# Performance work log

Hardware: AMD Instinct MI355X
Metric: run time of the kernel (lower is better)

## Reference

```python
import jax, jax.numpy as jnp
import numpy as np

B, L, D, H, S = 4, 4096, 1024, 16, 4
DH = D // H


def setup_inputs() -> dict:
    key = jax.random.key(0)
    ks = jax.random.split(key, 12)
    std = 0.02
    inp = {
        "x": jax.random.normal(ks[0], (B, L, D), jnp.float32),
        "scale_logits": jax.random.normal(ks[1], (S,), jnp.float32),
        "wq": jax.random.normal(ks[2], (D, D), jnp.float32) * std,
        "bq": jnp.zeros((D,), jnp.float32),
        "wk": jax.random.normal(ks[3], (D, D), jnp.float32) * std,
        "bk": jnp.zeros((D,), jnp.float32),
        "wv": jax.random.normal(ks[4], (D, D), jnp.float32) * std,
        "bv": jnp.zeros((D,), jnp.float32),
        "wo": jax.random.normal(ks[5], (D, D), jnp.float32) * std,
        "bo": jnp.zeros((D,), jnp.float32),
        "ws": jax.random.normal(ks[6], (S, D, D), jnp.float32) * std,  # per-scale Linear weights (out,in)
        "bs": jax.random.normal(ks[7], (S, D), jnp.float32) * std,
    }
    return inp


def reference(x, scale_logits, wq, bq, wk, bk, wv, bv, wo, bo, ws, bs):
    # q/k/v projections; kept flat (B,L,D) since the torch code re-flattens before scale proj
    qf = x @ wq.T + bq
    kf = x @ wk.T + bk
    vf = x @ wv.T + bv
    # per-scale linear projection, vectorized over scales: (B,S,L,D)
    sq = jnp.einsum('bld,sed->bsle', qf, ws) + bs[None, :, None, :]
    sk = jnp.einsum('bld,sed->bsle', kf, ws) + bs[None, :, None, :]
    sv = jnp.einsum('bld,sed->bsle', vf, ws) + bs[None, :, None, :]
    sq = sq.reshape(B, S, L, H, DH)
    sk = sk.reshape(B, S, L, H, DH)
    sv = sv.reshape(B, S, L, H, DH)
    # faithful to torch: matmul over last two dims of (B,L,H,dh) -> per-position
    # head-mixing scores of shape (B,S,L,H,H)
    scale = 1.0 / np.sqrt(DH).astype(np.float32)
    scores = jnp.einsum('bslhd,bslgd->bslhg', sq, sk) * scale
    attn = jax.nn.softmax(scores, axis=-1)
    out = jnp.einsum('bslhg,bslgd->bslhd', attn, sv)  # (B,S,L,H,DH)
    w = jax.nn.softmax(scale_logits, axis=0)  # (S,)
    combined = jnp.einsum('s,bslhd->blhd', w, out).reshape(B, L, D)
    return combined @ wo.T + bo
```

## Files before the change

### kernel.cpp

```cpp
#include <hip/hip_runtime.h>


typedef unsigned short u16;
typedef __attribute__((ext_vector_type(8))) short s16x8;
typedef __attribute__((ext_vector_type(8))) unsigned short u16x8;
typedef __attribute__((ext_vector_type(4))) float f32x4;

#define MM 16384
#define DDIM 1024
#define DDSQ 1048576ull

__device__ __forceinline__ u16 f2bf(float f) {
  unsigned u = __float_as_uint(f);
  u = (u + 0x7FFFu + ((u >> 16) & 1u)) >> 16;
  return (u16)u;
}
__device__ __forceinline__ float b2f(u16 b) {
  return __uint_as_float(((unsigned)b) << 16);
}
__device__ __forceinline__ void gload_lds16(const void* g, void* l) {
  __builtin_amdgcn_global_load_lds(
      (const __attribute__((address_space(1))) void*)g,
      (__attribute__((address_space(3))) void*)l, 16, 0, 0);
}

__global__ __launch_bounds__(256) void k_f32_to_bf16(
    const float* __restrict__ in, u16* __restrict__ out, int n4) {
  int i = blockIdx.x * 256 + threadIdx.x;
  if (i >= n4) return;
  float4 v = reinterpret_cast<const float4*>(in)[i];
  ushort4 o;
  o.x = f2bf(v.x); o.y = f2bf(v.y); o.z = f2bf(v.z); o.w = f2bf(v.w);
  reinterpret_cast<ushort4*>(out)[i] = o;
}

__global__ __launch_bounds__(256) void k_transpose_bf16(
    const float* __restrict__ wq, const float* __restrict__ wk,
    const float* __restrict__ wv, u16* __restrict__ out) {
  __shared__ float tile[32][33];
  const float* src = (blockIdx.z == 0) ? wq : (blockIdx.z == 1) ? wk : wv;
  u16* dst = out + (size_t)blockIdx.z * DDSQ;
  int tx = threadIdx.x, ty = threadIdx.y;
  int bx = blockIdx.x * 32, by = blockIdx.y * 32;
#pragma unroll
  for (int i = 0; i < 4; ++i)
    tile[ty + 8 * i][tx] = src[(size_t)(by + ty + 8 * i) * DDIM + bx + tx];
  __syncthreads();
#pragma unroll
  for (int i = 0; i < 4; ++i)
    dst[(size_t)(bx + ty + 8 * i) * DDIM + by + tx] = f2bf(tile[tx][ty + 8 * i]);
}

__global__ __launch_bounds__(256) void k_bias_fuse(
    const float* __restrict__ ws, const float* __restrict__ bq,
    const float* __restrict__ bk, const float* __restrict__ bv,
    const float* __restrict__ bs, float* __restrict__ bf) {
  int idx = blockIdx.y;
  int s = idx / 3, t = idx - s * 3;
  const float* bt = (t == 0) ? bq : (t == 1) ? bk : bv;
  int lane = threadIdx.x & 63, wid = threadIdx.x >> 6;
  int e = blockIdx.x * 4 + wid;
  const float* wr = ws + (size_t)s * DDSQ + (size_t)e * DDIM;
  float p = 0.f;
  for (int j = lane; j < DDIM; j += 64) p += wr[j] * bt[j];
#pragma unroll
  for (int off = 32; off > 0; off >>= 1) p += __shfl_xor(p, off);
  if (lane == 0) bf[idx * DDIM + e] = p + bs[s * DDIM + e];
}

template <typename OutT>
__global__ __launch_bounds__(256) void k_gemm_bt(
    const u16* __restrict__ A, const u16* __restrict__ B, OutT* __restrict__ C,
    const float* __restrict__ bias, int M, int N, int K,
    size_t za, size_t zb, size_t zc, size_t zbias, int zmode) {
  __shared__ u16 lds_a[128 * 32];
  __shared__ u16 lds_b[128 * 32];

  int z = blockIdx.x >> 3;
  int n_blk = blockIdx.x & 7;
  int m_blk = blockIdx.y;
  if (zmode == 1) { A += (size_t)(z / 3) * za; B += (size_t)(z % 3) * zb; }
  else            { A += (size_t)z * za;       B += (size_t)z * zb; }
  C += (size_t)z * zc;
  const float* biasz = bias ? (bias + (size_t)z * zbias) : nullptr;

  int m0 = m_blk * 128, n0 = n_blk * 128;
  int tid = threadIdx.x;
  int lane = tid & 63, wid = tid >> 6;
  int wm = wid >> 1, wn = wid & 1;

  f32x4 acc[4][4] = {};

  auto stage = [&](int k0) {
#pragma unroll
    for (int i = 0; i < 2; ++i) {
      int c = wid * 2 + i;
      int row = c * 16 + (lane >> 2);
      int col = (lane & 3) * 8;
      gload_lds16(A + (size_t)(m0 + row) * K + k0 + col, &lds_a[c * 512]);
      gload_lds16(B + (size_t)(n0 + row) * K + k0 + col, &lds_b[c * 512]);
    }
  };

  stage(0);
  int ar = (wm * 64 + (lane & 15)) * 32 + (lane >> 4) * 8;
  int br = (wn * 64 + (lane & 15)) * 32 + (lane >> 4) * 8;
  for (int k0 = 0;;) {
    __syncthreads();
    s16x8 af[4], bfr[4];
#pragma unroll
    for (int mi = 0; mi < 4; ++mi)
      af[mi] = *reinterpret_cast<const s16x8*>(&lds_a[ar + mi * 16 * 32]);
#pragma unroll
    for (int ni = 0; ni < 4; ++ni)
      bfr[ni] = *reinterpret_cast<const s16x8*>(&lds_b[br + ni * 16 * 32]);
#pragma unroll
    for (int mi = 0; mi < 4; ++mi)
#pragma unroll
      for (int ni = 0; ni < 4; ++ni)
        acc[mi][ni] = __builtin_amdgcn_mfma_f32_16x16x32_bf16(
            af[mi], bfr[ni], acc[mi][ni], 0, 0, 0);
    k0 += 32;
    if (k0 >= K) break;
    __syncthreads();
    stage(k0);
  }

#pragma unroll
  for (int mi = 0; mi < 4; ++mi) {
#pragma unroll
    for (int ni = 0; ni < 4; ++ni) {
      int colg = n0 + wn * 64 + ni * 16 + (lane & 15);
      float badd = biasz ? biasz[colg] : 0.f;
#pragma unroll
      for (int r = 0; r < 4; ++r) {
        int rowg = m0 + wm * 64 + mi * 16 + ((lane >> 4) << 2) + r;
        float v = acc[mi][ni][r] + badd;
        if constexpr (sizeof(OutT) == 2) C[(size_t)rowg * N + colg] = f2bf(v);
        else                             C[(size_t)rowg * N + colg] = v;
      }
    }
  }
}

template <typename OutT>
__global__ __launch_bounds__(512, 1) void k_gemm256(
    const u16* __restrict__ A, const u16* __restrict__ B, OutT* __restrict__ C,
    const float* __restrict__ bias, int M, int N, int K,
    size_t za, size_t zb, size_t zc, size_t zbias, int nbx) {
  __shared__ u16 lds[4][2][8192];

  int z = blockIdx.x / nbx;
  int nb = blockIdx.x - z * nbx;
  const u16* Ag = A + (size_t)z * za;
  const u16* Bg = B + (size_t)z * zb;
  OutT* Cg = C + (size_t)z * zc;
  const float* biasz = bias + (size_t)z * zbias;

  int m0 = blockIdx.y * 256, n0 = nb * 256;
  int tid = threadIdx.x;
  int lane = tid & 63, wid = tid >> 6;
  int wm = wid >> 2, wn = wid & 3;
  int NT = K >> 5;

  int scb = ((lane & 3) * 16) ^ (((lane >> 3) & 3) << 4);
  const char* srcA[2]; const char* srcB[2]; int ldsc[2];
#pragma unroll
  for (int r = 0; r < 2; ++r) {
    int c = r * 8 + wid;
    int row = c * 16 + (lane >> 2);
    srcA[r] = (const char*)Ag + ((size_t)(m0 + row) * K) * 2 + scb;
    srcB[r] = (const char*)Bg + ((size_t)(n0 + row) * K) * 2 + scb;
    ldsc[r] = c * 1024;
  }
  char* lbase = (char*)&lds[0][0][0];

  int fxor = ((lane >> 4) * 16) ^ (((lane >> 1) & 3) << 4);
  int aoff = (wm * 128 + (lane & 15)) * 64 + fxor;
  int boff = (wn * 64 + (lane & 15)) * 64 + fxor;

  f32x4 acc[8][4] = {};
  s16x8 cA0[4], cA1[4], cB[4];
  s16x8 nA0[4], nA1[4], nB[4];

#define STAGE_A(kt, rg)                                                   \
  {                                                                       \
    _Pragma("unroll") for (int r = 0; r < 2; ++r)                         \
        gload_lds16(srcA[r] + (size_t)(kt) * 64,                          \
                    lbase + (rg) * 32768 + ldsc[r]);                      \
  }
#define STAGE_B(kt, rg)                                                   \
  {                                                                       \
    _Pragma("unroll") for (int r = 0; r < 2; ++r)                         \
        gload_lds16(srcB[r] + (size_t)(kt) * 64,                          \
                    lbase + (rg) * 32768 + 16384 + ldsc[r]);              \
  }
#define SUBITER(C0, C1, CBv, N0, N1, NBv, tcur)                           \
  {                                                                       \
    asm volatile("s_waitcnt vmcnt(4)" ::: "memory");                      \
    asm volatile("s_barrier" ::: "memory");                               \
    int tn = (tcur) + 1 < NT ? (tcur) + 1 : NT - 1;                       \
    const char* bA = lbase + (tn & 3) * 32768;                            \
    const char* bB = bA + 16384;                                          \
    _Pragma("unroll") for (int i = 0; i < 4; ++i)                         \
        NBv[i] = *(const s16x8*)(bB + boff + i * 1024);                   \
    _Pragma("unroll") for (int i = 0; i < 4; ++i)                         \
        N0[i] = *(const s16x8*)(bA + aoff + i * 1024);                    \
    _Pragma("unroll") for (int i = 0; i < 4; ++i)                         \
        N1[i] = *(const s16x8*)(bA + aoff + 4096 + i * 1024);             \
    int ts = (tcur) + 3 < NT ? (tcur) + 3 : NT - 1;                       \
    int rgs = ((tcur) + 3) & 3;                                           \
    STAGE_A(ts, rgs); STAGE_B(ts, rgs);                                   \
    __builtin_amdgcn_s_setprio(1);                                        \
    _Pragma("unroll") for (int mi = 0; mi < 4; ++mi)                      \
      _Pragma("unroll") for (int ni = 0; ni < 4; ++ni)                    \
          acc[mi][ni] = __builtin_amdgcn_mfma_f32_16x16x32_bf16(          \
              C0[mi], CBv[ni], acc[mi][ni], 0, 0, 0);                     \
    _Pragma("unroll") for (int mi = 0; mi < 4; ++mi)                      \
      _Pragma("unroll") for (int ni = 0; ni < 4; ++ni)                    \
          acc[mi + 4][ni] = __builtin_amdgcn_mfma_f32_16x16x32_bf16(      \
              C1[mi], CBv[ni], acc[mi + 4][ni], 0, 0, 0);                 \
    __builtin_amdgcn_s_setprio(0);                                        \
  }

  STAGE_A(0, 0); STAGE_B(0, 0);
  STAGE_A(1, 1); STAGE_B(1, 1);
  STAGE_A(2, 2); STAGE_B(2, 2);
  asm volatile("s_waitcnt vmcnt(8)" ::: "memory");
  asm volatile("s_barrier" ::: "memory");
  {
    const char* bA = lbase;
    const char* bB = bA + 16384;
#pragma unroll
    for (int i = 0; i < 4; ++i) cB[i]  = *(const s16x8*)(bB + boff + i * 1024);
#pragma unroll
    for (int i = 0; i < 4; ++i) cA0[i] = *(const s16x8*)(bA + aoff + i * 1024);
#pragma unroll
    for (int i = 0; i < 4; ++i)
      cA1[i] = *(const s16x8*)(bA + aoff + 4096 + i * 1024);
  }

  for (int t = 0; t < NT; t += 2) {
    SUBITER(cA0, cA1, cB, nA0, nA1, nB, t);
    SUBITER(nA0, nA1, nB, cA0, cA1, cB, t + 1);
  }
#undef SUBITER
#undef STAGE_A
#undef STAGE_B

  asm volatile("s_waitcnt vmcnt(0)" ::: "memory");

#pragma unroll
  for (int mi = 0; mi < 8; ++mi) {
#pragma unroll
    for (int ni = 0; ni < 4; ++ni) {
      int colg = n0 + wn * 64 + ni * 16 + (lane & 15);
      float badd = biasz[colg];
#pragma unroll
      for (int r = 0; r < 4; ++r) {
        int rowg = m0 + wm * 128 + mi * 16 + ((lane >> 4) << 2) + r;
        float v = acc[mi][ni][r] + badd;
        if constexpr (sizeof(OutT) == 2) Cg[(size_t)rowg * N + colg] = f2bf(v);
        else                             Cg[(size_t)rowg * N + colg] = v;
      }
    }
  }
}

__global__ __launch_bounds__(256) void k_attn_all(
    const u16* __restrict__ proj, u16* __restrict__ outbf,
    const float* __restrict__ sl, int rows) {
  __shared__ u16 kv[4][2][2][1024];
  int lane = threadIdx.x & 63, wid = threadIdx.x >> 6;
  int row = blockIdx.x * 4 + wid;
  int h = lane >> 2, dq = lane & 3;
  int doff = h * 64 + dq * 16;

  float l0 = sl[0], l1 = sl[1], l2 = sl[2], l3 = sl[3];
  float lm = fmaxf(fmaxf(l0, l1), fmaxf(l2, l3));
  float e0 = __expf(l0 - lm), e1 = __expf(l1 - lm), e2 = __expf(l2 - lm),
        e3 = __expf(l3 - lm);
  float esum = e0 + e1 + e2 + e3;
  float wsc4[4] = {e0 / esum, e1 / esum, e2 / esum, e3 / esum};

#define KV_ISSUE(s, buf)                                                   \
  {                                                                        \
    const u16* kr = proj + ((size_t)(3 * (s) + 1) * rows + row) * DDIM;    \
    const u16* vr = proj + ((size_t)(3 * (s) + 2) * rows + row) * DDIM;    \
    gload_lds16(kr + lane * 8,       &kv[wid][buf][0][0]);                 \
    gload_lds16(kr + 512 + lane * 8, &kv[wid][buf][0][512]);               \
    gload_lds16(vr + lane * 8,       &kv[wid][buf][1][0]);                 \
    gload_lds16(vr + 512 + lane * 8, &kv[wid][buf][1][512]);               \
  }

  KV_ISSUE(0, 0);

  float acc[16];
#pragma unroll
  for (int i = 0; i < 16; ++i) acc[i] = 0.f;

  for (int s = 0; s < 4; ++s) {
    int buf = s & 1;

    const u16* qr = proj + ((size_t)(3 * s) * rows + row) * DDIM + doff;
    u16x8 q0 = *reinterpret_cast<const u16x8*>(qr);
    u16x8 q1 = *reinterpret_cast<const u16x8*>(qr + 8);

    if (s < 3) KV_ISSUE(s + 1, buf ^ 1);

    if (s < 3) asm volatile("s_waitcnt vmcnt(6)" ::: "memory");
    else       asm volatile("s_waitcnt vmcnt(0)" ::: "memory");

    float qf[16];
#pragma unroll
    for (int i = 0; i < 8; ++i) {
      qf[i]     = b2f(q0[i]) * 0.125f;
      qf[8 + i] = b2f(q1[i]) * 0.125f;
    }

    float sc[16];
#pragma unroll
    for (int g = 0; g < 16; ++g) {
      const u16* kp = &kv[wid][buf][0][g * 64 + dq * 16];
      u16x8 k0 = *reinterpret_cast<const u16x8*>(kp);
      u16x8 k1 = *reinterpret_cast<const u16x8*>(kp + 8);
      float d = 0.f;
#pragma unroll
      for (int i = 0; i < 8; ++i) d = fmaf(qf[i], b2f(k0[i]), d);
#pragma unroll
      for (int i = 0; i < 8; ++i) d = fmaf(qf[8 + i], b2f(k1[i]), d);
      d += __shfl_xor(d, 1);
      d += __shfl_xor(d, 2);
      sc[g] = d;
    }

    float mx = sc[0];
#pragma unroll
    for (int g = 1; g < 16; ++g) mx = fmaxf(mx, sc[g]);
    float sum = 0.f;
#pragma unroll
    for (int g = 0; g < 16; ++g) { sc[g] = __expf(sc[g] - mx); sum += sc[g]; }
    float inv = wsc4[s] / sum;
#pragma unroll
    for (int g = 0; g < 16; ++g) sc[g] *= inv;

#pragma unroll
    for (int g = 0; g < 16; ++g) {
      float a = sc[g];
      const u16* vp = &kv[wid][buf][1][g * 64 + dq * 16];
      u16x8 v0 = *reinterpret_cast<const u16x8*>(vp);
      u16x8 v1 = *reinterpret_cast<const u16x8*>(vp + 8);
#pragma unroll
      for (int i = 0; i < 8; ++i) {
        acc[i]     = fmaf(a, b2f(v0[i]), acc[i]);
        acc[8 + i] = fmaf(a, b2f(v1[i]), acc[8 + i]);
      }
    }
  }
#undef KV_ISSUE

  u16* op = outbf + (size_t)row * DDIM + doff;
  u16x8 o0, o1;
#pragma unroll
  for (int i = 0; i < 8; ++i) {
    o0[i] = f2bf(acc[i]);
    o1[i] = f2bf(acc[8 + i]);
  }
  *reinterpret_cast<u16x8*>(op) = o0;
  *reinterpret_cast<u16x8*>(op + 8) = o1;
}

extern "C" void kernel_launch(void* const* d_in, const int* in_sizes, int n_in,
                              void* d_out, int out_size, void* d_ws,
                              size_t ws_size, hipStream_t stream) {
  const float* x  = (const float*)d_in[0];
  const float* sl = (const float*)d_in[1];
  const float* wq = (const float*)d_in[2];
  const float* bq = (const float*)d_in[3];
  const float* wk = (const float*)d_in[4];
  const float* bk = (const float*)d_in[5];
  const float* wv = (const float*)d_in[6];
  const float* bv = (const float*)d_in[7];
  const float* wo = (const float*)d_in[8];
  const float* bo = (const float*)d_in[9];
  const float* ws = (const float*)d_in[10];
  const float* bs = (const float*)d_in[11];
  float* out = (float*)d_out;

  char* wsb = (char*)d_ws;
  size_t off = 0;
  u16* xbf    = (u16*)(wsb + off); off += (size_t)MM * DDIM * 2;
  u16* wfus   = (u16*)(wsb + off); off += 12ull * DDSQ * 2;
  u16* wobf   = (u16*)(wsb + off); off += DDSQ * 2;
  float* bfus = (float*)(wsb + off); off += 65536;
  u16* combc  = (u16*)(wsb + off); off += (size_t)MM * DDIM * 2;
  char* dynr  = wsb + off;
  size_t fixed = off;

  int chunk = 4096;
  while (chunk > 1024 && fixed + (size_t)12 * chunk * DDIM * 2 > ws_size)
    chunk >>= 1;
  u16* projc = (u16*)dynr;
  u16* wtT  = (u16*)dynr;
  u16* wsbf = (u16*)(dynr + 3ull * DDSQ * 2);

  int n4;
  n4 = MM * DDIM / 4;
  k_f32_to_bf16<<<(n4 + 255) / 256, 256, 0, stream>>>(x, xbf, n4);
  n4 = (int)(4 * DDSQ / 4);
  k_f32_to_bf16<<<(n4 + 255) / 256, 256, 0, stream>>>(ws, wsbf, n4);
  n4 = (int)(DDSQ / 4);
  k_f32_to_bf16<<<(n4 + 255) / 256, 256, 0, stream>>>(wo, wobf, n4);

  k_transpose_bf16<<<dim3(32, 32, 3), dim3(32, 8), 0, stream>>>(wq, wk, wv, wtT);
  k_bias_fuse<<<dim3(256, 12), 256, 0, stream>>>(ws, bq, bk, bv, bs, bfus);

  k_gemm_bt<u16><<<dim3(96, 8), 256, 0, stream>>>(
      wsbf, wtT, wfus, nullptr, 1024, 1024, 1024, DDSQ, DDSQ, DDSQ, 0, 1);

  int nchunks = MM / chunk;
  for (int c = 0; c < nchunks; ++c) {
    const u16* xa = xbf + (size_t)c * chunk * DDIM;
    k_gemm256<u16><<<dim3(48, chunk / 256), 512, 0, stream>>>(
        xa, wfus, projc, bfus, chunk, 1024, 1024,
        0, DDSQ, (size_t)chunk * DDIM, DDIM, 4);
    k_attn_all<<<dim3(chunk / 4), 256, 0, stream>>>(
        projc, combc + (size_t)c * chunk * DDIM, sl, chunk);
  }

  k_gemm256<float><<<dim3(4, 64), 512, 0, stream>>>(
      combc, wobf, out, bo, MM, 1024, 1024, 0, 0, 0, 0, 4);
}
```

Baseline: 690.0 us.

## Add eight-phase pipelined bf16 GEMM kernel for fused scale projections

Adds a new 256x256-tile bf16 GEMM kernel and uses it for the large fused Q/K/V scale projection GEMM. K is split into half-tiles across double-buffered LDS, with direct global-to-LDS loads for the next tiles issued between the MFMA phases. It also adds explicit barriers, waitcnt, priority bumps around MFMA and XOR-swizzled LDS addressing. The intent is to hide global memory latency behind tensor-core work. The cost is 128KB of LDS per block (one block per CU) and more barriers per K step.

```diff
diff --git a/kernel.cpp b/kernel.cpp
--- a/kernel.cpp
+++ b/kernel.cpp
@@ -267,6 +267,158 @@
   }
 }
 
+__global__ __launch_bounds__(512, 1) void k_gemm8p(
+    const u16* __restrict__ A, const u16* __restrict__ B, u16* __restrict__ C,
+    const float* __restrict__ bias, int M, int N, int K,
+    size_t za, size_t zb, size_t zc, size_t zbias, int nbx) {
+  __shared__ char lds[131072];
+
+  int z = blockIdx.x / nbx;
+  int nb = blockIdx.x - z * nbx;
+  const u16* Ag = A + (size_t)z * za;
+  const u16* Bg = B + (size_t)z * zb;
+  u16* Cg = C + (size_t)z * zc;
+  const float* biasz = bias + (size_t)z * zbias;
+
+  int m0 = blockIdx.y * 256, n0 = nb * 256;
+  int tid = threadIdx.x;
+  int lane = tid & 63, wid = tid >> 6;
+  int wm = wid >> 2, wn = wid & 3;
+  int NT = K >> 6;
+
+  int scb = ((lane & 3) * 16) ^ (((lane >> 3) & 3) << 4);
+  const char* srcA[2]; const char* srcB[2]; int ldsc[2];
+#pragma unroll
+  for (int r = 0; r < 2; ++r) {
+    int c = r * 8 + wid;
+    int row = c * 16 + (lane >> 2);
+    srcA[r] = (const char*)Ag + ((size_t)(m0 + row) * K) * 2 + scb;
+    srcB[r] = (const char*)Bg + ((size_t)(n0 + row) * K) * 2 + scb;
+    ldsc[r] = c * 1024;
+  }
+
+  int fxor = ((lane >> 4) * 16) ^ (((lane >> 1) & 3) << 4);
+  int aoffb = (wm * 128 + (lane & 15)) * 64 + fxor;
+  int boffb = (wn * 64 + (lane & 15)) * 64 + fxor;
+
+  f32x4 acc[2][4][4] = {};
+  s16x8 fb0[4], fb1[4];
+
+#define ST8(srcX, kt, kh, dst)                                            \
+  {                                                                       \
+    _Pragma("unroll") for (int r = 0; r < 2; ++r)                         \
+        gload_lds16(srcX[r] + (size_t)(kt) * 128 + (kh) * 64,             \
+                    lds + (dst) + ldsc[r]);                               \
+  }
+#define BAR8 asm volatile("s_barrier" ::: "memory")
+#define LGKM0                                                             \
+  {                                                                       \
+    asm volatile("s_waitcnt lgkmcnt(0)" ::: "memory");                    \
+    __builtin_amdgcn_sched_barrier(0);                                    \
+  }
+#define RDA8(fa, bo, kh, ch)                                              \
+  {                                                                       \
+    const char* ra_ = lds + (bo) + (kh) * 16384;                          \
+    _Pragma("unroll") for (int mf = 0; mf < 4; ++mf)                      \
+        fa[mf] = *(const s16x8*)(ra_ + aoffb + (ch) * 4096 + mf * 1024);  \
+  }
+#define RDB8(fb, bo, kh)                                                  \
+  {                                                                       \
+    const char* rb_ = lds + (bo) + 32768 + (kh) * 16384;                  \
+    _Pragma("unroll") for (int nf = 0; nf < 4; ++nf)                      \
+        fb[nf] = *(const s16x8*)(rb_ + boffb + nf * 1024);                \
+  }
+#define MFMA16(ch, fa, fb)                                                \
+  {                                                                       \
+    __builtin_amdgcn_s_setprio(1);                                        \
+    _Pragma("unroll") for (int mf = 0; mf < 4; ++mf)                      \
+      _Pragma("unroll") for (int nf = 0; nf < 4; ++nf)                    \
+          acc[ch][mf][nf] = __builtin_amdgcn_mfma_f32_16x16x32_bf16(      \
+              fa[mf], fb[nf], acc[ch][mf][nf], 0, 0, 0);                  \
+    __builtin_amdgcn_s_setprio(0);                                        \
+  }
+
+  ST8(srcA, 0, 0, 0);
+  ST8(srcB, 0, 0, 32768);
+  ST8(srcA, 0, 1, 16384);
+  ST8(srcB, 0, 1, 49152);
+  {
+    int t1 = (NT > 1) ? 1 : 0;
+    ST8(srcA, t1, 0, 65536 + 0);
+    ST8(srcB, t1, 0, 65536 + 32768);
+  }
+  asm volatile("s_waitcnt vmcnt(4)" ::: "memory");
+  BAR8;
+
+  for (int t = 0; t < NT; ++t) {
+    int bo  = (t & 1) << 16;
+    int bo1 = ((t & 1) ^ 1) << 16;
+    int tn1 = (t + 1 < NT) ? t + 1 : NT - 1;
+    int tn2 = (t + 2 < NT) ? t + 2 : NT - 1;
+
+    {
+      s16x8 fa[4];
+      RDB8(fb0, bo, 0);
+      RDA8(fa, bo, 0, 0);
+      ST8(srcA, tn1, 1, bo1 + 16384);
+      BAR8; LGKM0;
+      MFMA16(0, fa, fb0);
+      BAR8;
+    }
+    {
+      s16x8 fa[4];
+      RDA8(fa, bo, 0, 1);
+      ST8(srcB, tn1, 1, bo1 + 49152);
+      BAR8; LGKM0;
+      MFMA16(1, fa, fb0);
+      BAR8;
+    }
+    {
+      s16x8 fa[4];
+      RDB8(fb1, bo, 1);
+      RDA8(fa, bo, 1, 0);
+      ST8(srcA, tn2, 0, bo + 0);
+      BAR8; LGKM0;
+      MFMA16(0, fa, fb1);
+      BAR8;
+    }
+    {
+      s16x8 fa[4];
+      RDA8(fa, bo, 1, 1);
+      ST8(srcB, tn2, 0, bo + 32768);
+      BAR8; LGKM0;
+      MFMA16(1, fa, fb1);
+      asm volatile("s_waitcnt vmcnt(4)" ::: "memory");
+      BAR8;
+    }
+  }
+#undef ST8
+#undef BAR8
+#undef LGKM0
+#undef RDA8
+#undef RDB8
+#undef MFMA16
+
+  asm volatile("s_waitcnt vmcnt(0)" ::: "memory");
+
+#pragma unroll
+  for (int ch = 0; ch < 2; ++ch) {
+#pragma unroll
+    for (int mf = 0; mf < 4; ++mf) {
+#pragma unroll
+      for (int nf = 0; nf < 4; ++nf) {
+        int colg = n0 + wn * 64 + nf * 16 + (lane & 15);
+        float badd = biasz[colg];
+#pragma unroll
+        for (int r = 0; r < 4; ++r) {
+          int rowg = m0 + wm * 128 + ch * 64 + mf * 16 + ((lane >> 4) << 2) + r;
+          Cg[(size_t)rowg * N + colg] = f2bf(acc[ch][mf][nf][r] + badd);
+        }
+      }
+    }
+  }
+}
+
 __global__ __launch_bounds__(256) void k_attn_all(
     const u16* __restrict__ proj, u16* __restrict__ outbf,
     const float* __restrict__ sl, int rows) {
@@ -421,7 +573,7 @@
   int nchunks = MM / chunk;
   for (int c = 0; c < nchunks; ++c) {
     const u16* xa = xbf + (size_t)c * chunk * DDIM;
-    k_gemm256<u16><<<dim3(48, chunk / 256), 512, 0, stream>>>(
+    k_gemm8p<<<dim3(48, chunk / 256), 512, 0, stream>>>(
         xa, wfus, projc, bfus, chunk, 1024, 1024,
         0, DDSQ, (size_t)chunk * DDIM, DDIM, 4);
     k_attn_all<<<dim3(chunk / 4), 256, 0, stream>>>(
```

After: 711.8 us. +3.2%, slower.
